# Performance work log

Measured on AMD Instinct MI355X. Metric: run time of the kernel, lower is better.

## Reference

```python
import jax, jax.numpy as jnp
import numpy as np


def setup_inputs() -> dict:
    key = jax.random.key(0)
    k1, k2, k3, k4 = jax.random.split(key, 4)
    B, M, S, Q = 128, 200, 20, 20
    H, V, D = 3, 50000, 128  # max_hops, num_vocab, embedding_dim
    story = jax.random.randint(k1, (B, M, S), 0, V)
    query = jax.random.randint(k2, (B, Q), 0, V)
    # (max_hops+1) embedding tables, init normal(0, 0.1) as in torch code
    E = jax.random.normal(k3, (H + 1, V, D), dtype=jnp.float32) * 0.1
    # (max_hops+1) temporal encodings [max_story_size, D], normal(0, 0.1)
    T = jax.random.normal(k4, (H + 1, M, D), dtype=jnp.float32) * 0.1
    return {"story": story, "query": query, "E": E, "T": T}


def reference(story, query, E, T):
    max_hops = E.shape[0] - 1
    # u1 = sum over query tokens of B-embedding (hop-0 table)
    u = jnp.sum(E[0][query], axis=1)  # [B, D]
    for hop in range(max_hops):
        # memory: A-embed story, sum over words, add temporal encoding
        m = jnp.sum(E[hop][story], axis=2) + T[hop]        # [B, M, D]
        # attention over memories (legacy F.softmax on 2D -> dim=1)
        uTm = jnp.einsum('bmd,bd->bm', m, u)               # [B, M]
        proba = jax.nn.softmax(uTm, axis=1)
        # output memory representation
        c = jnp.sum(E[hop + 1][story], axis=2) + T[hop + 1]  # [B, M, D]
        o = jnp.einsum('bm,bmd->bd', proba, c)             # [B, D]
        u = u + o
    ahat = u @ E[-1].T  # [B, V]
    return ahat, jax.nn.softmax(ahat, axis=1)
```

## Files before the change

### kernel.cpp

```cpp
#include <hip/hip_runtime.h>
#include <float.h>


constexpr int Bn = 128;
constexpr int Mn = 200;
constexpr int Sn = 20;
constexpr int Qn = 20;
constexpr int Hn = 3;
constexpr int Vn = 50000;
constexpr int Dn = 128;
constexpr int CH = 100;

constexpr int GTILE = 128;
constexpr int NT    = (Vn + GTILE - 1) / GTILE;
constexpr int SMCHK = 10;

constexpr int TSTR = 130;

constexpr size_t MSUM_ELEMS = (size_t)(Hn + 1) * Bn * Mn * Dn;
constexpr size_t SMWS_ELEMS = (size_t)NT * Bn * 2;

__global__ __launch_bounds__(256)
void msum_kernel(const int* __restrict__ story, const float* __restrict__ E,
                 const float* __restrict__ T, float* __restrict__ msum) {
    int slot = threadIdx.x >> 5;
    int l    = threadIdx.x & 31;
    int row  = blockIdx.x * 8 + slot;
    int t    = row / (Bn * Mn);
    int rem  = row - t * (Bn * Mn);
    int b    = rem / Mn;
    int m    = rem - b * Mn;

    const int* st = story + (b * Mn + m) * Sn;
    const float4* Tv = (const float4*)(T) + (size_t)(t * Mn + m) * 32;
    const float4* Et = (const float4*)(E) + (size_t)t * Vn * 32;

    int idx[Sn];
    #pragma unroll
    for (int s = 0; s < Sn; ++s) idx[s] = st[s];

    float4 e[Sn];
    #pragma unroll
    for (int s = 0; s < Sn; ++s) e[s] = Et[(size_t)idx[s] * 32 + l];

    float4 acc = Tv[l];
    #pragma unroll
    for (int s = 0; s < Sn; ++s) {
        acc.x += e[s].x; acc.y += e[s].y; acc.z += e[s].z; acc.w += e[s].w;
    }
    ((float4*)msum)[(size_t)row * 32 + l] = acc;
}

__global__ __launch_bounds__(1024)
void hops_kernel(const int* __restrict__ query, const float* __restrict__ E,
                 const float* __restrict__ msum, float* __restrict__ ufin) {
    __shared__ __align__(16) float tileA[Mn * TSTR];
    __shared__ float u[Dn];
    __shared__ float sc[Mn];
    __shared__ float op[1024];
    __shared__ float red[16];
    __shared__ float bc[2];

    const int b    = blockIdx.x;
    const int tid  = threadIdx.x;
    const int wave = tid >> 6;
    const int lane = tid & 63;
    const int d    = tid & (Dn - 1);
    const int g    = tid >> 7;
    const int dq   = tid >> 8;
    const int mm   = tid & 255;

    auto stage = [&](int t) {
        const float* src = msum + ((size_t)t * Bn + b) * (size_t)(Mn * Dn);
        float2 vbuf[13];
        #pragma unroll
        for (int k = 0; k < 13; ++k) {
            int r = wave + 16 * k;
            if (r < Mn)
                vbuf[k] = *(const float2*)(src + (size_t)r * Dn + 2 * lane);
        }
        #pragma unroll
        for (int k = 0; k < 13; ++k) {
            int r = wave + 16 * k;
            if (r < Mn)
                *(float2*)(tileA + r * TSTR + 2 * lane) = vbuf[k];
        }
    };

    if (tid < Dn) {
        float acc = 0.f;
        const int* q = query + b * Qn;
        #pragma unroll
        for (int j = 0; j < Qn; ++j)
            acc += E[(size_t)q[j] * Dn + tid];
        u[tid] = acc;
    }
    stage(0);
    __syncthreads();

    for (int hop = 0; hop < Hn; ++hop) {
        if (mm < Mn) {
            float p = 0.f;
            #pragma unroll
            for (int i = 0; i < 32; ++i)
                p += tileA[mm * TSTR + dq * 32 + i] * u[dq * 32 + i];
            op[dq * Mn + mm] = p;
        }
        __syncthreads();

        float v = -FLT_MAX;
        if (tid < Mn)
            v = op[tid] + op[Mn + tid] + op[2 * Mn + tid] + op[3 * Mn + tid];
        float mx = v;
        #pragma unroll
        for (int off = 32; off; off >>= 1) mx = fmaxf(mx, __shfl_down(mx, off, 64));
        if (lane == 0) red[wave] = mx;
        __syncthreads();
        if (tid == 0) {
            float m0 = red[0];
            #pragma unroll
            for (int i = 1; i < 16; ++i) m0 = fmaxf(m0, red[i]);
            bc[0] = m0;
        }
        __syncthreads();
        float rmax = bc[0];
        float e = (tid < Mn) ? __expf(v - rmax) : 0.f;
        float sm = e;
        #pragma unroll
        for (int off = 32; off; off >>= 1) sm += __shfl_down(sm, off, 64);
        if (lane == 0) red[wave] = sm;
        __syncthreads();
        if (tid == 0) {
            float s = 0.f;
            #pragma unroll
            for (int i = 0; i < 16; ++i) s += red[i];
            bc[1] = s;
        }
        __syncthreads();
        float inv = 1.f / bc[1];
        if (tid < Mn) sc[tid] = e * inv;

        stage(hop + 1);
        __syncthreads();

        float acc = 0.f;
        #pragma unroll
        for (int k = 0; k < 25; ++k) {
            int m = g + 8 * k;
            acc += sc[m] * tileA[m * TSTR + d];
        }
        op[g * Dn + d] = acc;
        __syncthreads();
        if (tid < Dn) {
            float s = 0.f;
            #pragma unroll
            for (int i = 0; i < 8; ++i) s += op[i * Dn + tid];
            u[tid] += s;
        }
        __syncthreads();
    }
    if (tid < Dn) ufin[b * Dn + tid] = u[tid];
}

__global__ __launch_bounds__(1024)
void hops_fused_kernel(const int* __restrict__ story, const int* __restrict__ query,
                       const float* __restrict__ E, const float* __restrict__ T,
                       float* __restrict__ ufin) {
    __shared__ __align__(16) float tile[CH * Dn];
    __shared__ float u[Dn];
    __shared__ float sc[Mn];
    __shared__ float op[8 * Dn];
    __shared__ float red[16];
    __shared__ float bc[2];

    const int b    = blockIdx.x;
    const int tid  = threadIdx.x;
    const int wave = tid >> 6;
    const int lane = tid & 63;
    const int d    = tid & (Dn - 1);
    const int g    = tid >> 7;
    const int slot = tid >> 5;
    const int l    = tid & 31;
    const int* st  = story + b * (Mn * Sn);

    if (tid < Dn) {
        float acc = 0.f;
        const int* q = query + b * Qn;
        #pragma unroll
        for (int j = 0; j < Qn; ++j)
            acc += E[(size_t)q[j] * Dn + tid];
        u[tid] = acc;
    }

    auto build = [&](int t, int base) {
        const float4* Et = (const float4*)(E) + (size_t)t * Vn * 32;
        const float4* Tt = (const float4*)(T) + (size_t)t * Mn * 32;
        for (int m = base + slot; m < base + CH; m += 32) {
            const int* sm = st + m * Sn;
            float4 acc = Tt[(size_t)m * 32 + l];
            #pragma unroll
            for (int s = 0; s < Sn; ++s) {
                float4 e = Et[(size_t)sm[s] * 32 + l];
                acc.x += e.x; acc.y += e.y; acc.z += e.z; acc.w += e.w;
            }
            ((float4*)tile)[(m - base) * 32 + l] = acc;
        }
    };
    auto scores = [&](int base) {
        for (int m = base + wave; m < base + CH; m += 16) {
            float p = tile[(m - base) * Dn + lane]      * u[lane]
                    + tile[(m - base) * Dn + lane + 64] * u[lane + 64];
            #pragma unroll
            for (int off = 32; off; off >>= 1) p += __shfl_down(p, off, 64);
            if (lane == 0) sc[m] = p;
        }
    };

    for (int hop = 0; hop < Hn; ++hop) {
        if (hop == 0) {
            build(0, 0);  __syncthreads(); scores(0);  __syncthreads();
            build(0, CH); __syncthreads(); scores(CH); __syncthreads();
        } else {
            scores(CH); __syncthreads();
            build(hop, 0); __syncthreads(); scores(0); __syncthreads();
        }

        float v = (tid < Mn) ? sc[tid] : -FLT_MAX;
        float mx = v;
        #pragma unroll
        for (int off = 32; off; off >>= 1) mx = fmaxf(mx, __shfl_down(mx, off, 64));
        if (lane == 0) red[wave] = mx;
        __syncthreads();
        if (tid == 0) {
            float m0 = red[0];
            #pragma unroll
            for (int i = 1; i < 16; ++i) m0 = fmaxf(m0, red[i]);
            bc[0] = m0;
        }
        __syncthreads();
        float rmax = bc[0];
        float e = (tid < Mn) ? __expf(v - rmax) : 0.f;
        float sm = e;
        #pragma unroll
        for (int off = 32; off; off >>= 1) sm += __shfl_down(sm, off, 64);
        if (lane == 0) red[wave] = sm;
        __syncthreads();
        if (tid == 0) {
            float s = 0.f;
            #pragma unroll
            for (int i = 0; i < 16; ++i) s += red[i];
            bc[1] = s;
        }
        __syncthreads();
        float inv = 1.f / bc[1];
        if (tid < Mn) sc[tid] = e * inv;

        float oacc = 0.f;
        build(hop + 1, 0);
        __syncthreads();
        for (int m = g; m < CH; m += 8)
            oacc += sc[m] * tile[m * Dn + d];
        __syncthreads();
        build(hop + 1, CH);
        __syncthreads();
        for (int m = CH + g; m < 2 * CH; m += 8)
            oacc += sc[m] * tile[(m - CH) * Dn + d];
        op[g * Dn + d] = oacc;
        __syncthreads();
        if (tid < Dn) {
            float s = 0.f;
            #pragma unroll
            for (int i = 0; i < 8; ++i) s += op[i * Dn + tid];
            u[tid] += s;
        }
        __syncthreads();
    }

    if (tid < Dn) ufin[b * Dn + tid] = u[tid];
}

constexpr int KC   = 32;
constexpr int LSTR = 140;
__device__ __forceinline__ int ldsCol(int c) { return c + 4 * (c >> 5); }

__global__ __launch_bounds__(256)
void ahat_gemm_kernel(const float* __restrict__ E, const float* __restrict__ ufin,
                      float* __restrict__ out, float* __restrict__ ws2) {
    __shared__ __align__(16) float uA[KC * LSTR];
    __shared__ __align__(16) float eB[KC * LSTR];
    const float* E3 = E + (size_t)Hn * Vn * Dn;

    const int tid   = threadIdx.x;
    const int tr    = tid & 15;
    const int tc    = tid >> 4;
    const int vbase = blockIdx.x * GTILE;

    const int f4 = tid & 7;
    const int rr = tid >> 3;

    float acc[8][8];
    #pragma unroll
    for (int i = 0; i < 8; ++i)
        #pragma unroll
        for (int j = 0; j < 8; ++j) acc[i][j] = 0.f;

    for (int kb = 0; kb < Dn; kb += KC) {
        #pragma unroll
        for (int i = 0; i < 4; ++i) {
            int r   = rr + 32 * i;
            int col = ldsCol(r);
            float4 uv = *(const float4*)(ufin + (size_t)r * Dn + kb + f4 * 4);
            uA[(f4 * 4 + 0) * LSTR + col] = uv.x;
            uA[(f4 * 4 + 1) * LSTR + col] = uv.y;
            uA[(f4 * 4 + 2) * LSTR + col] = uv.z;
            uA[(f4 * 4 + 3) * LSTR + col] = uv.w;
        }
        #pragma unroll
        for (int i = 0; i < 4; ++i) {
            int r  = rr + 32 * i;
            int vg = vbase + r; if (vg > Vn - 1) vg = Vn - 1;
            int col = ldsCol(r);
            float4 ev = *(const float4*)(E3 + (size_t)vg * Dn + kb + f4 * 4);
            eB[(f4 * 4 + 0) * LSTR + col] = ev.x;
            eB[(f4 * 4 + 1) * LSTR + col] = ev.y;
            eB[(f4 * 4 + 2) * LSTR + col] = ev.z;
            eB[(f4 * 4 + 3) * LSTR + col] = ev.w;
        }
        __syncthreads();
        const int ca = ldsCol(tr * 8);
        const int cb = ldsCol(tc * 8);
        #pragma unroll 2
        for (int k = 0; k < KC; ++k) {
            float4 a0 = *(const float4*)&uA[k * LSTR + ca];
            float4 a1 = *(const float4*)&uA[k * LSTR + ca + 4];
            float4 b0 = *(const float4*)&eB[k * LSTR + cb];
            float4 b1 = *(const float4*)&eB[k * LSTR + cb + 4];
            float av[8] = {a0.x, a0.y, a0.z, a0.w, a1.x, a1.y, a1.z, a1.w};
            float bv[8] = {b0.x, b0.y, b0.z, b0.w, b1.x, b1.y, b1.z, b1.w};
            #pragma unroll
            for (int i = 0; i < 8; ++i)
                #pragma unroll
                for (int j = 0; j < 8; ++j)
                    acc[i][j] += av[i] * bv[j];
        }
        __syncthreads();
    }

    const int  v0    = vbase + tc * 8;
    const bool valid = v0 < Vn;
    if (valid) {
        #pragma unroll
        for (int i = 0; i < 8; ++i) {
            int bb = tr * 8 + i;
            *(float4*)(out + (size_t)bb * Vn + v0) =
                make_float4(acc[i][0], acc[i][1], acc[i][2], acc[i][3]);
            *(float4*)(out + (size_t)bb * Vn + v0 + 4) =
                make_float4(acc[i][4], acc[i][5], acc[i][6], acc[i][7]);
        }
    }

    if (ws2) {
        #pragma unroll
        for (int i = 0; i < 8; ++i) {
            float tm = -FLT_MAX, ts = 0.f;
            if (valid) {
                #pragma unroll
                for (int j = 0; j < 8; ++j) tm = fmaxf(tm, acc[i][j]);
                #pragma unroll
                for (int j = 0; j < 8; ++j) ts += __expf(acc[i][j] - tm);
            }
            uA[tc * 128 + tr * 8 + i] = tm;
            eB[tc * 128 + tr * 8 + i] = ts;
        }
        __syncthreads();
        if (tid < Bn) {
            float M = -FLT_MAX;
            #pragma unroll
            for (int t = 0; t < 16; ++t) M = fmaxf(M, uA[t * 128 + tid]);
            float S = 0.f;
            #pragma unroll
            for (int t = 0; t < 16; ++t)
                S += eB[t * 128 + tid] * __expf(uA[t * 128 + tid] - M);
            float2* w = (float2*)ws2;
            w[(size_t)blockIdx.x * Bn + tid] = make_float2(M, S);
        }
    }
}

__global__ __launch_bounds__(256)
void softmax_merge_kernel(const float* __restrict__ ahat, const float* __restrict__ ws2,
                          float* __restrict__ osm) {
    __shared__ float redm[4], reds[4];
    __shared__ float bcM, bcI;

    const int ck   = blockIdx.x;
    const int b    = blockIdx.y;
    const int tid  = threadIdx.x;
    const int wave = tid >> 6;
    const int lane = tid & 63;

    float m = -FLT_MAX, s = 0.f;
    const float2* w = (const float2*)ws2;
    for (int i = tid; i < NT; i += 256) {
        float2 p = w[(size_t)i * Bn + b];
        float nm = fmaxf(m, p.x);
        s = s * __expf(m - nm) + p.y * __expf(p.x - nm);
        m = nm;
    }
    #pragma unroll
    for (int off = 32; off; off >>= 1) {
        float mo = __shfl_down(m, off, 64);
        float so = __shfl_down(s, off, 64);
        float nm = fmaxf(m, mo);
        s = s * __expf(m - nm) + so * __expf(mo - nm);
        m = nm;
    }
    if (lane == 0) { redm[wave] = m; reds[wave] = s; }
    __syncthreads();
    if (tid == 0) {
        float M = redm[0];
        #pragma unroll
        for (int i = 1; i < 4; ++i) M = fmaxf(M, redm[i]);
        float S = 0.f;
        #pragma unroll
        for (int i = 0; i < 4; ++i) S += reds[i] * __expf(redm[i] - M);
        bcM = M; bcI = 1.f / S;
    }
    __syncthreads();
    const float M   = bcM;
    const float inv = bcI;

    constexpr int C4 = Vn / SMCHK / 4;
    const float4* row  = (const float4*)(ahat + (size_t)b * Vn) + (size_t)ck * C4;
    float4*       orow = (float4*)(osm + (size_t)b * Vn) + (size_t)ck * C4;
    for (int v = tid; v < C4; v += 256) {
        float4 x = row[v];
        orow[v] = make_float4(__expf(x.x - M) * inv, __expf(x.y - M) * inv,
                              __expf(x.z - M) * inv, __expf(x.w - M) * inv);
    }
}

__global__ __launch_bounds__(1024)
void softmax_kernel(const float* __restrict__ ahat, float* __restrict__ osm) {
    __shared__ float redm[16];
    __shared__ float reds[16];
    __shared__ float bc2[2];

    int b    = blockIdx.x;
    int tid  = threadIdx.x;
    int wave = tid >> 6;
    int lane = tid & 63;

    const float4* row  = (const float4*)(ahat + (size_t)b * Vn);
    float4*       orow = (float4*)(osm + (size_t)b * Vn);
    constexpr int N4 = Vn / 4;

    float m = -FLT_MAX, s = 0.f;
    for (int v = tid; v < N4; v += 1024) {
        float4 x = row[v];
        float cm = fmaxf(fmaxf(x.x, x.y), fmaxf(x.z, x.w));
        if (cm > m) { s *= __expf(m - cm); m = cm; }
        s += __expf(x.x - m) + __expf(x.y - m) + __expf(x.z - m) + __expf(x.w - m);
    }
    #pragma unroll
    for (int off = 32; off; off >>= 1) {
        float mo = __shfl_down(m, off, 64);
        float so = __shfl_down(s, off, 64);
        float nm = fmaxf(m, mo);
        s = s * __expf(m - nm) + so * __expf(mo - nm);
        m = nm;
    }
    if (lane == 0) { redm[wave] = m; reds[wave] = s; }
    __syncthreads();
    if (tid == 0) {
        float M = redm[0];
        #pragma unroll
        for (int i = 1; i < 16; ++i) M = fmaxf(M, redm[i]);
        float S = 0.f;
        #pragma unroll
        for (int i = 0; i < 16; ++i) S += reds[i] * __expf(redm[i] - M);
        bc2[0] = M; bc2[1] = 1.f / S;
    }
    __syncthreads();
    float rmax = bc2[0];
    float inv  = bc2[1];

    for (int v = tid; v < N4; v += 1024) {
        float4 x = row[v];
        orow[v] = make_float4(__expf(x.x - rmax) * inv, __expf(x.y - rmax) * inv,
                              __expf(x.z - rmax) * inv, __expf(x.w - rmax) * inv);
    }
}

extern "C" void kernel_launch(void* const* d_in, const int* in_sizes, int n_in,
                              void* d_out, int out_size, void* d_ws, size_t ws_size,
                              hipStream_t stream) {
    const int*   story = (const int*)d_in[0];
    const int*   query = (const int*)d_in[1];
    const float* E     = (const float*)d_in[2];
    const float* T     = (const float*)d_in[3];

    float* out  = (float*)d_out;
    float* ufin = out + (size_t)Bn * Vn;

    const bool haveMsum = ws_size >= MSUM_ELEMS * sizeof(float);
    const bool haveSm   = ws_size >= (MSUM_ELEMS + SMWS_ELEMS) * sizeof(float);
    float* msum = (float*)d_ws;
    float* ws2  = haveSm ? ((float*)d_ws + MSUM_ELEMS) : nullptr;

    if (haveMsum) {
        msum_kernel<<<(Hn + 1) * Bn * Mn / 8, 256, 0, stream>>>(story, E, T, msum);
        hops_kernel<<<Bn, 1024, 0, stream>>>(query, E, msum, ufin);
    } else {
        hops_fused_kernel<<<Bn, 1024, 0, stream>>>(story, query, E, T, ufin);
    }

    ahat_gemm_kernel<<<NT, 256, 0, stream>>>(E, ufin, out, ws2);

    if (ws2) {
        softmax_merge_kernel<<<dim3(SMCHK, Bn), 256, 0, stream>>>(
            out, ws2, out + (size_t)Bn * Vn);
    } else {
        softmax_kernel<<<Bn, 1024, 0, stream>>>(out, out + (size_t)Bn * Vn);
    }
}
```

Measured before the change: 324.6 us.

## Prefetch next hop's memory tile during score computation; nontemporal msum stores

In the hops kernel, the global loads of the next hop's memory matrix now start at the top of each hop, before the dot-product scoring, so their latency overlaps that compute. The values are written into shared memory after the first barrier, replacing the old stage call that sat after the softmax. In msum_kernel the embedding loads are moved into the accumulation loop, and the result is written with a nontemporal store. The cost is 26 extra live registers per thread in a 1024-thread block, and the nontemporal hint may reduce L2 reuse when hops_kernel later reads msum.

```diff
diff --git a/kernel.cpp b/kernel.cpp
--- a/kernel.cpp
+++ b/kernel.cpp
@@ -19,6 +19,8 @@
 
 constexpr size_t MSUM_ELEMS = (size_t)(Hn + 1) * Bn * Mn * Dn;
 constexpr size_t SMWS_ELEMS = (size_t)NT * Bn * 2;
+
+typedef float f32x4 __attribute__((ext_vector_type(4)));
 
 __global__ __launch_bounds__(256)
 void msum_kernel(const int* __restrict__ story, const float* __restrict__ E,
@@ -39,16 +41,14 @@
     #pragma unroll
     for (int s = 0; s < Sn; ++s) idx[s] = st[s];
 
-    float4 e[Sn];
-    #pragma unroll
-    for (int s = 0; s < Sn; ++s) e[s] = Et[(size_t)idx[s] * 32 + l];
-
     float4 acc = Tv[l];
     #pragma unroll
     for (int s = 0; s < Sn; ++s) {
-        acc.x += e[s].x; acc.y += e[s].y; acc.z += e[s].z; acc.w += e[s].w;
-    }
-    ((float4*)msum)[(size_t)row * 32 + l] = acc;
+        float4 e = Et[(size_t)idx[s] * 32 + l];
+        acc.x += e.x; acc.y += e.y; acc.z += e.z; acc.w += e.w;
+    }
+    f32x4 av = {acc.x, acc.y, acc.z, acc.w};
+    __builtin_nontemporal_store(av, (f32x4*)msum + (size_t)row * 32 + l);
 }
 
 __global__ __launch_bounds__(1024)
@@ -70,8 +70,8 @@
     const int dq   = tid >> 8;
     const int mm   = tid & 255;
 
-    auto stage = [&](int t) {
-        const float* src = msum + ((size_t)t * Bn + b) * (size_t)(Mn * Dn);
+    {
+        const float* src = msum + ((size_t)0 * Bn + b) * (size_t)(Mn * Dn);
         float2 vbuf[13];
         #pragma unroll
         for (int k = 0; k < 13; ++k) {
@@ -85,7 +85,7 @@
             if (r < Mn)
                 *(float2*)(tileA + r * TSTR + 2 * lane) = vbuf[k];
         }
-    };
+    }
 
     if (tid < Dn) {
         float acc = 0.f;
@@ -95,10 +95,20 @@
             acc += E[(size_t)q[j] * Dn + tid];
         u[tid] = acc;
     }
-    stage(0);
     __syncthreads();
 
     for (int hop = 0; hop < Hn; ++hop) {
+        float2 vbuf[13];
+        {
+            const float* src = msum + ((size_t)(hop + 1) * Bn + b) * (size_t)(Mn * Dn);
+            #pragma unroll
+            for (int k = 0; k < 13; ++k) {
+                int r = wave + 16 * k;
+                if (r < Mn)
+                    vbuf[k] = *(const float2*)(src + (size_t)r * Dn + 2 * lane);
+            }
+        }
+
         if (mm < Mn) {
             float p = 0.f;
             #pragma unroll
@@ -107,6 +117,13 @@
             op[dq * Mn + mm] = p;
         }
         __syncthreads();
+
+        #pragma unroll
+        for (int k = 0; k < 13; ++k) {
+            int r = wave + 16 * k;
+            if (r < Mn)
+                *(float2*)(tileA + r * TSTR + 2 * lane) = vbuf[k];
+        }
 
         float v = -FLT_MAX;
         if (tid < Mn)
@@ -139,8 +156,6 @@
         __syncthreads();
         float inv = 1.f / bc[1];
         if (tid < Mn) sc[tid] = e * inv;
-
-        stage(hop + 1);
         __syncthreads();
 
         float acc = 0.f;
```

Result: no change. 329.3 us (+1.5%).
